# Kernel optimization log

Hardware: AMD Instinct MI355X
Metric: run time of the kernel (lower is better)

The kernel has to match this reference:

```python
import jax, jax.numpy as jnp
import numpy as np
import math

B, N, IN_DIM, OUT_DIM, H = 8, 1024, 256, 256, 8
D_K = OUT_DIM // H


def setup_inputs() -> dict:
    key = jax.random.key(0)
    ks = jax.random.split(key, 12)
    s_in = 1.0 / math.sqrt(IN_DIM)
    s_out = 1.0 / math.sqrt(OUT_DIM)
    return {
        "X": jax.random.normal(ks[0], (B, N, IN_DIM), jnp.float32),
        "A": jax.random.randint(ks[1], (B, N, N), 0, 2, jnp.int32),
        "D": jax.random.uniform(ks[2], (B, N, N), jnp.float32),
        "W_q": jax.random.uniform(ks[3], (IN_DIM, OUT_DIM), jnp.float32, -s_in, s_in),
        "b_q": jax.random.uniform(ks[4], (OUT_DIM,), jnp.float32, -s_in, s_in),
        "W_k": jax.random.uniform(ks[5], (IN_DIM, OUT_DIM), jnp.float32, -s_in, s_in),
        "b_k": jax.random.uniform(ks[6], (OUT_DIM,), jnp.float32, -s_in, s_in),
        "W_v": jax.random.uniform(ks[7], (IN_DIM, OUT_DIM), jnp.float32, -s_in, s_in),
        "b_v": jax.random.uniform(ks[8], (OUT_DIM,), jnp.float32, -s_in, s_in),
        "W_o": jax.random.uniform(ks[9], (OUT_DIM, OUT_DIM), jnp.float32, -s_out, s_out),
        "b_o": jax.random.uniform(ks[10], (OUT_DIM,), jnp.float32, -s_out, s_out),
        "dist_scale": jnp.array(1.0, jnp.float32),
    }


def reference(X, A, D, W_q, b_q, W_k, b_k, W_v, b_v, W_o, b_o, dist_scale):
    b, n, _ = X.shape
    # Projections -> [B, H, N, d_k]
    Q = (X @ W_q + b_q).reshape(b, n, H, D_K).transpose(0, 2, 1, 3)
    K = (X @ W_k + b_k).reshape(b, n, H, D_K).transpose(0, 2, 1, 3)
    V = (X @ W_v + b_v).reshape(b, n, H, D_K).transpose(0, 2, 1, 3)
    scores = jnp.einsum("bhqd,bhkd->bhqk", Q, K) / jnp.sqrt(jnp.float32(D_K))
    scores = scores - dist_scale * D[:, None, :, :]
    scores = jnp.where(A[:, None, :, :] <= 0, jnp.float32(-1e9), scores)
    attn = jax.nn.softmax(scores, axis=-1)  # dropout is identity in eval mode
    out = jnp.einsum("bhqk,bhkd->bhqd", attn, V)
    out = out.transpose(0, 2, 1, 3).reshape(b, n, H * D_K)
    return out @ W_o + b_o
```

## Files before the change

### kernel.cpp

```cpp
#include <hip/hip_runtime.h>


typedef __bf16 bf16x8 __attribute__((ext_vector_type(8)));
typedef float f32x4 __attribute__((ext_vector_type(4)));
typedef int i32x4 __attribute__((ext_vector_type(4)));
typedef unsigned short u16x8 __attribute__((ext_vector_type(8)));
typedef _Float16 f16x8 __attribute__((ext_vector_type(8)));

#define DEV static __device__ __forceinline__

#define LOG2E 1.4426950408889634f
#define QSCALE 0.2550351062f

DEV unsigned short f2bf(float f) {
  union { float f; unsigned u; } x; x.f = f;
  unsigned r = x.u + 0x7fffu + ((x.u >> 16) & 1u);
  return (unsigned short)(r >> 16);
}

DEV unsigned short f2h(float f) {
  _Float16 h = (_Float16)f;
  unsigned short u;
  __builtin_memcpy(&u, &h, 2);
  return u;
}

DEV float h2f(unsigned short u) {
  _Float16 h;
  __builtin_memcpy(&h, &u, 2);
  return (float)h;
}

DEV f32x4 mfma16(bf16x8 a, bf16x8 b, f32x4 c) {
  return __builtin_amdgcn_mfma_f32_16x16x32_bf16(a, b, c, 0, 0, 0);
}

DEV bf16x8 ldfrag(const unsigned short* p) {
  return *reinterpret_cast<const bf16x8*>(p);
}

__global__ __launch_bounds__(256) void k_prep(
    const float* __restrict__ X, const int* __restrict__ A,
    const float* __restrict__ D, const float* __restrict__ dscale,
    const float* __restrict__ Wq, const float* __restrict__ Wk,
    const float* __restrict__ Wv, const float* __restrict__ Wo,
    unsigned short* __restrict__ Xbf, unsigned short* __restrict__ Wt,
    unsigned short* __restrict__ Bias) {
  const int tid = blockIdx.x * 256 + threadIdx.x;
  const int NB4 = (8 * 1024 * 1024) / 4;
  const int NX4 = (8192 * 256) / 4;
  if (tid < NB4) {
    const i32x4 a4 = reinterpret_cast<const i32x4*>(A)[tid];
    const f32x4 d4 = reinterpret_cast<const f32x4*>(D)[tid];
    const float c = -dscale[0] * LOG2E;
    ushort4 o;
    unsigned short* op = (unsigned short*)&o;
    #pragma unroll
    for (int i = 0; i < 4; ++i)
      op[i] = f2h(a4[i] <= 0 ? -60000.0f : c * d4[i]);
    reinterpret_cast<ushort4*>(Bias)[tid] = o;
  } else if (tid < NB4 + NX4) {
    const int t = tid - NB4;
    float4 v = reinterpret_cast<const float4*>(X)[t];
    ushort4 o;
    o.x = f2bf(v.x); o.y = f2bf(v.y); o.z = f2bf(v.z); o.w = f2bf(v.w);
    reinterpret_cast<ushort4*>(Xbf)[t] = o;
  } else {
    int t = tid - NB4 - NX4;
    int mat = t >> 16;
    int e = t & 65535;
    int n = e >> 8, k = e & 255;
    const float* W = (mat == 0) ? Wq : (mat == 1) ? Wk : (mat == 2) ? Wv : Wo;
    Wt[t] = f2bf(W[k * 256 + n]);
  }
}

__global__ __launch_bounds__(256, 2) void k_qkv(
    const unsigned short* __restrict__ Xbf, const unsigned short* __restrict__ Wt,
    const float* __restrict__ bq, const float* __restrict__ bk,
    const float* __restrict__ bv,
    unsigned short* __restrict__ Qb, unsigned short* __restrict__ Kb,
    unsigned short* __restrict__ Vt) {
  const int lane = threadIdx.x & 63;
  const int w = threadIdx.x >> 6;
  const int lr = lane & 15, lg = lane >> 4;
  const int mat = blockIdx.y >> 2;
  const int nloc = (blockIdx.y & 3) * 64 + w * 16;
  const int mbase = blockIdx.x << 8;

  const unsigned short* Wm = Wt + mat * 65536;
  const float* bias = (mat == 0) ? bq : (mat == 1) ? bk : bv;

  bf16x8 bfr[8];
  #pragma unroll
  for (int ks = 0; ks < 8; ++ks)
    bfr[ks] = ldfrag(Wm + (nloc + lr) * 256 + ks * 32 + lg * 8);
  const float bb = bias[nloc + lr];
  const int cm = nloc + lr;
  const int hh = cm >> 5, d = cm & 31;

  for (int mt = 0; mt < 16; ++mt) {
    const int m0 = mbase + mt * 16;
    bf16x8 a[8];
    #pragma unroll
    for (int ks = 0; ks < 8; ++ks)
      a[ks] = ldfrag(Xbf + (m0 + lr) * 256 + ks * 32 + lg * 8);
    f32x4 acc = {0.f, 0.f, 0.f, 0.f};
    #pragma unroll
    for (int ks = 0; ks < 8; ++ks)
      acc = mfma16(a[ks], bfr[ks], acc);

    if (mat == 2) {
      ushort4 vv;
      unsigned short* vp = (unsigned short*)&vv;
      #pragma unroll
      for (int i = 0; i < 4; ++i) vp[i] = f2bf(acc[i] + bb);
      const int row = m0 + lg * 4;
      const int bidx = row >> 10, nn = row & 1023;
      *reinterpret_cast<ushort4*>(&Vt[(((bidx * 8 + hh) * 32) + d) * 1024 + nn]) = vv;
    } else if (mat == 0) {
      #pragma unroll
      for (int i = 0; i < 4; ++i) {
        const int row = m0 + lg * 4 + i;
        const int bidx = row >> 10, nn = row & 1023;
        Qb[(((bidx * 8 + hh) * 1024) + nn) * 32 + d] = f2bf((acc[i] + bb) * QSCALE);
      }
    } else {
      #pragma unroll
      for (int i = 0; i < 4; ++i) {
        const int row = m0 + lg * 4 + i;
        const int bidx = row >> 10, nn = row & 1023;
        Kb[(((bidx * 8 + hh) * 1024) + nn) * 32 + d] = f2bf(acc[i] + bb);
      }
    }
  }
}

__global__ __launch_bounds__(512, 2) void k_attn(
    const unsigned short* __restrict__ Qb, const unsigned short* __restrict__ Kb,
    const unsigned short* __restrict__ Vt, const unsigned short* __restrict__ Bias,
    unsigned short* __restrict__ AO) {
  __shared__ alignas(16) unsigned short Klds[1024 * 32];
  __shared__ alignas(16) unsigned short Vlds[32 * 1024];
  __shared__ alignas(16) unsigned short Sbuf[8][16][72];

  const int tid = threadIdx.x;
  const int lane = tid & 63;
  const int w = tid >> 6;
  const int lr = lane & 15, lg = lane >> 4;
  const int bi = blockIdx.x;
  const int b = bi & 7;
  const int j = bi >> 3;
  const int h = j >> 2, qq = j & 3;
  const int q0w = qq * 256 + w * 32;

  const unsigned short* Kg = Kb + ((size_t)(b * 8 + h) << 15);
  const unsigned short* Vg = Vt + ((size_t)(b * 8 + h) << 15);
  const unsigned short* Qh = Qb + ((size_t)(b * 8 + h) << 15);

  #pragma unroll
  for (int p = 0; p < 8; ++p) {
    const int c = tid + p * 512;
    const int row = c >> 2, seg = c & 3;
    const u16x8 v = *reinterpret_cast<const u16x8*>(Kg + c * 8);
    *reinterpret_cast<u16x8*>(&Klds[row * 32 + ((seg ^ (row & 3)) << 3)]) = v;
  }
  #pragma unroll
  for (int p = 0; p < 8; ++p) {
    const int c = tid + p * 512;
    const int row = c >> 7, ch = c & 127;
    const u16x8 v = *reinterpret_cast<const u16x8*>(Vg + c * 8);
    *reinterpret_cast<u16x8*>(&Vlds[row * 1024 + ((ch ^ (row & 7)) << 3)]) = v;
  }

  bf16x8 qf[2];
  qf[0] = ldfrag(Qh + (q0w + lr) * 32 + lg * 8);
  qf[1] = ldfrag(Qh + (q0w + 16 + lr) * 32 + lg * 8);
  const unsigned short* Br0 = Bias + ((size_t)b << 20) + (size_t)(q0w + lr) * 1024;
  const unsigned short* Br1 = Br0 + (size_t)16 * 1024;

  u16x8 bc[2][2], bn[2][2];
  #pragma unroll
  for (int fr = 0; fr < 2; ++fr) {
    bc[0][fr] = *reinterpret_cast<const u16x8*>(Br0 + fr * 32 + lg * 8);
    bc[1][fr] = *reinterpret_cast<const u16x8*>(Br1 + fr * 32 + lg * 8);
  }

  __syncthreads();

  f32x4 o[2][2];
  #pragma unroll
  for (int s = 0; s < 2; ++s)
    #pragma unroll
    for (int dh = 0; dh < 2; ++dh) o[s][dh] = f32x4{0.f, 0.f, 0.f, 0.f};
  float ps[2] = {0.f, 0.f};

  for (int t = 0; t < 16; ++t) {
    const int k0 = t << 6;
    if (t < 15) {
      #pragma unroll
      for (int fr = 0; fr < 2; ++fr) {
        bn[0][fr] = *reinterpret_cast<const u16x8*>(Br0 + k0 + 64 + fr * 32 + lg * 8);
        bn[1][fr] = *reinterpret_cast<const u16x8*>(Br1 + k0 + 64 + fr * 32 + lg * 8);
      }
    }

    bf16x8 kf[4];
    #pragma unroll
    for (int st = 0; st < 4; ++st) {
      const int row = k0 + st * 16 + lr;
      kf[st] = *reinterpret_cast<const bf16x8*>(
          &Klds[row * 32 + ((lg ^ (lr & 3)) << 3)]);
    }
    bf16x8 vf[2][2];
    #pragma unroll
    for (int dh = 0; dh < 2; ++dh)
      #pragma unroll
      for (int fr = 0; fr < 2; ++fr) {
        const int row = dh * 16 + lr;
        const int ch = t * 8 + ((fr * 4 + lg) ^ (lr & 7));
        vf[dh][fr] = *reinterpret_cast<const bf16x8*>(&Vlds[row * 1024 + ch * 8]);
      }

    #pragma unroll
    for (int s = 0; s < 2; ++s) {
      const f32x4 zz = {0.f, 0.f, 0.f, 0.f};
      f32x4 sv[4];
      #pragma unroll
      for (int st = 0; st < 4; ++st)
        sv[st] = mfma16(kf[st], qf[s], zz);

      #pragma unroll
      for (int st = 0; st < 4; ++st) {
        ushort4 sw;
        unsigned short* sp = (unsigned short*)&sw;
        #pragma unroll
        for (int i = 0; i < 4; ++i) sp[i] = f2h(sv[st][i]);
        *reinterpret_cast<ushort4*>(&Sbuf[w][lr][st * 16 + lg * 4]) = sw;
      }

      #pragma unroll
      for (int fr = 0; fr < 2; ++fr) {
        const f16x8 sf = *reinterpret_cast<const f16x8*>(&Sbuf[w][lr][fr * 32 + lg * 8]);
        const unsigned short* bp = (const unsigned short*)&bc[s][fr];
        float p8[8];
        float psl = 0.f;
        #pragma unroll
        for (int i = 0; i < 8; ++i) {
          p8[i] = exp2f((float)sf[i] + h2f(bp[i]));
          psl += p8[i];
        }
        ps[s] += psl;
        bf16x8 pf;
        #pragma unroll
        for (int i = 0; i < 8; ++i) pf[i] = (__bf16)p8[i];
        o[s][0] = mfma16(vf[0][fr], pf, o[s][0]);
        o[s][1] = mfma16(vf[1][fr], pf, o[s][1]);
      }
    }

    #pragma unroll
    for (int s = 0; s < 2; ++s)
      #pragma unroll
      for (int fr = 0; fr < 2; ++fr)
        bc[s][fr] = bn[s][fr];
  }

  #pragma unroll
  for (int s = 0; s < 2; ++s) {
    float psum = ps[s];
    psum += __shfl_xor(psum, 16);
    psum += __shfl_xor(psum, 32);
    const float linv = 1.0f / psum;
    ushort4 r0, r1;
    unsigned short* r0p = (unsigned short*)&r0;
    unsigned short* r1p = (unsigned short*)&r1;
    #pragma unroll
    for (int i = 0; i < 4; ++i) {
      r0p[i] = f2bf(o[s][0][i] * linv);
      r1p[i] = f2bf(o[s][1][i] * linv);
    }
    const int row = (b << 10) + q0w + s * 16 + lr;
    *reinterpret_cast<ushort4*>(&AO[row * 256 + h * 32 + lg * 4]) = r0;
    *reinterpret_cast<ushort4*>(&AO[row * 256 + h * 32 + 16 + lg * 4]) = r1;
  }
}

__global__ __launch_bounds__(256, 2) void k_oproj(
    const unsigned short* __restrict__ AO, const unsigned short* __restrict__ Wto,
    const float* __restrict__ bo, float* __restrict__ out) {
  const int lane = threadIdx.x & 63;
  const int w = threadIdx.x >> 6;
  const int lr = lane & 15, lg = lane >> 4;
  const int c0 = blockIdx.y * 64 + w * 16;
  const int mbase = blockIdx.x << 7;

  bf16x8 bfr[8];
  #pragma unroll
  for (int ks = 0; ks < 8; ++ks)
    bfr[ks] = ldfrag(Wto + (c0 + lr) * 256 + ks * 32 + lg * 8);
  const float bb = bo[c0 + lr];

  for (int mt = 0; mt < 8; ++mt) {
    const int m0 = mbase + mt * 16;
    bf16x8 a[8];
    #pragma unroll
    for (int ks = 0; ks < 8; ++ks)
      a[ks] = ldfrag(AO + (m0 + lr) * 256 + ks * 32 + lg * 8);
    f32x4 acc = {0.f, 0.f, 0.f, 0.f};
    #pragma unroll
    for (int ks = 0; ks < 8; ++ks)
      acc = mfma16(a[ks], bfr[ks], acc);
    #pragma unroll
    for (int i = 0; i < 4; ++i) {
      const int row = m0 + lg * 4 + i;
      out[row * 256 + c0 + lr] = acc[i] + bb;
    }
  }
}

extern "C" void kernel_launch(void* const* d_in, const int* in_sizes, int n_in,
                              void* d_out, int out_size, void* d_ws, size_t ws_size,
                              hipStream_t stream) {
  const float* X   = (const float*)d_in[0];
  const int*   A   = (const int*)d_in[1];
  const float* D   = (const float*)d_in[2];
  const float* Wq  = (const float*)d_in[3];
  const float* bq  = (const float*)d_in[4];
  const float* Wk  = (const float*)d_in[5];
  const float* bk  = (const float*)d_in[6];
  const float* Wv  = (const float*)d_in[7];
  const float* bv  = (const float*)d_in[8];
  const float* Wo  = (const float*)d_in[9];
  const float* bo  = (const float*)d_in[10];
  const float* dsc = (const float*)d_in[11];
  float* out = (float*)d_out;

  unsigned short* ws = (unsigned short*)d_ws;
  unsigned short* Xbf  = ws;
  unsigned short* Wt   = ws + 2097152;
  unsigned short* Qb   = ws + 2359296;
  unsigned short* Kb   = ws + 4456448;
  unsigned short* Vt   = ws + 6553600;
  unsigned short* Bias = ws + 8650752;
  unsigned short* AO   = Xbf;

  hipLaunchKernelGGL(k_prep, dim3(11264), dim3(256), 0, stream,
                     X, A, D, dsc, Wq, Wk, Wv, Wo, Xbf, Wt, Bias);
  hipLaunchKernelGGL(k_qkv, dim3(32, 12), dim3(256), 0, stream,
                     Xbf, Wt, bq, bk, bv, Qb, Kb, Vt);
  hipLaunchKernelGGL(k_attn, dim3(256), dim3(512), 0, stream,
                     Qb, Kb, Vt, Bias, AO);
  hipLaunchKernelGGL(k_oproj, dim3(64, 4), dim3(256), 0, stream,
                     AO, Wt + 196608, bo, out);
}
```

Measured before the change: 99.94 us.

## Switch pipeline to fp16 MFMA with packed conversions and MFMA row sums

Moves all intermediates and matrix cores from bf16 to fp16 and replaces manual bf16 rounding with packed cvt_pkrtz conversions. In attention, the score-plus-bias add is done in packed fp16 and the softmax denominator is accumulated by an extra MFMA against a ones vector instead of scalar adds and cross-lane shuffles. This is meant to cut VALU conversion and reduction work in the inner loop. The trade-offs are one extra MFMA per fragment and fp16's narrower range with round-toward-zero conversion, which may cost accuracy.

```diff
diff --git a/kernel.cpp b/kernel.cpp
--- a/kernel.cpp
+++ b/kernel.cpp
@@ -1,22 +1,16 @@
 #include <hip/hip_runtime.h>
 
 
-typedef __bf16 bf16x8 __attribute__((ext_vector_type(8)));
+typedef _Float16 f16x8 __attribute__((ext_vector_type(8)));
+typedef __fp16 h16x2 __attribute__((ext_vector_type(2)));
 typedef float f32x4 __attribute__((ext_vector_type(4)));
 typedef int i32x4 __attribute__((ext_vector_type(4)));
 typedef unsigned short u16x8 __attribute__((ext_vector_type(8)));
-typedef _Float16 f16x8 __attribute__((ext_vector_type(8)));
 
 #define DEV static __device__ __forceinline__
 
 #define LOG2E 1.4426950408889634f
 #define QSCALE 0.2550351062f
-
-DEV unsigned short f2bf(float f) {
-  union { float f; unsigned u; } x; x.f = f;
-  unsigned r = x.u + 0x7fffu + ((x.u >> 16) & 1u);
-  return (unsigned short)(r >> 16);
-}
 
 DEV unsigned short f2h(float f) {
   _Float16 h = (_Float16)f;
@@ -25,18 +19,12 @@
   return u;
 }
 
-DEV float h2f(unsigned short u) {
-  _Float16 h;
-  __builtin_memcpy(&h, &u, 2);
-  return (float)h;
-}
-
-DEV f32x4 mfma16(bf16x8 a, bf16x8 b, f32x4 c) {
-  return __builtin_amdgcn_mfma_f32_16x16x32_bf16(a, b, c, 0, 0, 0);
-}
-
-DEV bf16x8 ldfrag(const unsigned short* p) {
-  return *reinterpret_cast<const bf16x8*>(p);
+DEV f32x4 mfma16h(f16x8 a, f16x8 b, f32x4 c) {
+  return __builtin_amdgcn_mfma_f32_16x16x32_f16(a, b, c, 0, 0, 0);
+}
+
+DEV f16x8 ldfragh(const unsigned short* p) {
+  return *reinterpret_cast<const f16x8*>(p);
 }
 
 __global__ __launch_bounds__(256) void k_prep(
@@ -44,7 +32,7 @@
     const float* __restrict__ D, const float* __restrict__ dscale,
     const float* __restrict__ Wq, const float* __restrict__ Wk,
     const float* __restrict__ Wv, const float* __restrict__ Wo,
-    unsigned short* __restrict__ Xbf, unsigned short* __restrict__ Wt,
+    unsigned short* __restrict__ Xh, unsigned short* __restrict__ Wt,
     unsigned short* __restrict__ Bias) {
   const int tid = blockIdx.x * 256 + threadIdx.x;
   const int NB4 = (8 * 1024 * 1024) / 4;
@@ -62,21 +50,22 @@
   } else if (tid < NB4 + NX4) {
     const int t = tid - NB4;
     float4 v = reinterpret_cast<const float4*>(X)[t];
-    ushort4 o;
-    o.x = f2bf(v.x); o.y = f2bf(v.y); o.z = f2bf(v.z); o.w = f2bf(v.w);
-    reinterpret_cast<ushort4*>(Xbf)[t] = o;
+    union { h16x2 h2[2]; ushort4 u; } o;
+    o.h2[0] = __builtin_amdgcn_cvt_pkrtz(v.x, v.y);
+    o.h2[1] = __builtin_amdgcn_cvt_pkrtz(v.z, v.w);
+    reinterpret_cast<ushort4*>(Xh)[t] = o.u;
   } else {
     int t = tid - NB4 - NX4;
     int mat = t >> 16;
     int e = t & 65535;
     int n = e >> 8, k = e & 255;
     const float* W = (mat == 0) ? Wq : (mat == 1) ? Wk : (mat == 2) ? Wv : Wo;
-    Wt[t] = f2bf(W[k * 256 + n]);
+    Wt[t] = f2h(W[k * 256 + n]);
   }
 }
 
 __global__ __launch_bounds__(256, 2) void k_qkv(
-    const unsigned short* __restrict__ Xbf, const unsigned short* __restrict__ Wt,
+    const unsigned short* __restrict__ Xh, const unsigned short* __restrict__ Wt,
     const float* __restrict__ bq, const float* __restrict__ bk,
     const float* __restrict__ bv,
     unsigned short* __restrict__ Qb, unsigned short* __restrict__ Kb,
@@ -91,46 +80,45 @@
   const unsigned short* Wm = Wt + mat * 65536;
   const float* bias = (mat == 0) ? bq : (mat == 1) ? bk : bv;
 
-  bf16x8 bfr[8];
+  f16x8 bfr[8];
   #pragma unroll
   for (int ks = 0; ks < 8; ++ks)
-    bfr[ks] = ldfrag(Wm + (nloc + lr) * 256 + ks * 32 + lg * 8);
+    bfr[ks] = ldfragh(Wm + (nloc + lr) * 256 + ks * 32 + lg * 8);
   const float bb = bias[nloc + lr];
   const int cm = nloc + lr;
   const int hh = cm >> 5, d = cm & 31;
 
   for (int mt = 0; mt < 16; ++mt) {
     const int m0 = mbase + mt * 16;
-    bf16x8 a[8];
+    f16x8 a[8];
     #pragma unroll
     for (int ks = 0; ks < 8; ++ks)
-      a[ks] = ldfrag(Xbf + (m0 + lr) * 256 + ks * 32 + lg * 8);
+      a[ks] = ldfragh(Xh + (m0 + lr) * 256 + ks * 32 + lg * 8);
     f32x4 acc = {0.f, 0.f, 0.f, 0.f};
     #pragma unroll
     for (int ks = 0; ks < 8; ++ks)
-      acc = mfma16(a[ks], bfr[ks], acc);
+      acc = mfma16h(a[ks], bfr[ks], acc);
 
     if (mat == 2) {
-      ushort4 vv;
-      unsigned short* vp = (unsigned short*)&vv;
-      #pragma unroll
-      for (int i = 0; i < 4; ++i) vp[i] = f2bf(acc[i] + bb);
+      union { h16x2 h2[2]; ushort4 u; } vv;
+      vv.h2[0] = __builtin_amdgcn_cvt_pkrtz(acc[0] + bb, acc[1] + bb);
+      vv.h2[1] = __builtin_amdgcn_cvt_pkrtz(acc[2] + bb, acc[3] + bb);
       const int row = m0 + lg * 4;
       const int bidx = row >> 10, nn = row & 1023;
-      *reinterpret_cast<ushort4*>(&Vt[(((bidx * 8 + hh) * 32) + d) * 1024 + nn]) = vv;
+      *reinterpret_cast<ushort4*>(&Vt[(((bidx * 8 + hh) * 32) + d) * 1024 + nn]) = vv.u;
     } else if (mat == 0) {
       #pragma unroll
       for (int i = 0; i < 4; ++i) {
         const int row = m0 + lg * 4 + i;
         const int bidx = row >> 10, nn = row & 1023;
-        Qb[(((bidx * 8 + hh) * 1024) + nn) * 32 + d] = f2bf((acc[i] + bb) * QSCALE);
+        Qb[(((bidx * 8 + hh) * 1024) + nn) * 32 + d] = f2h((acc[i] + bb) * QSCALE);
       }
     } else {
       #pragma unroll
       for (int i = 0; i < 4; ++i) {
         const int row = m0 + lg * 4 + i;
         const int bidx = row >> 10, nn = row & 1023;
-        Kb[(((bidx * 8 + hh) * 1024) + nn) * 32 + d] = f2bf(acc[i] + bb);
+        Kb[(((bidx * 8 + hh) * 1024) + nn) * 32 + d] = f2h(acc[i] + bb);
       }
     }
   }
@@ -173,9 +161,9 @@
     *reinterpret_cast<u16x8*>(&Vlds[row * 1024 + ((ch ^ (row & 7)) << 3)]) = v;
   }
 
-  bf16x8 qf[2];
-  qf[0] = ldfrag(Qh + (q0w + lr) * 32 + lg * 8);
-  qf[1] = ldfrag(Qh + (q0w + 16 + lr) * 32 + lg * 8);
+  f16x8 qf[2];
+  qf[0] = ldfragh(Qh + (q0w + lr) * 32 + lg * 8);
+  qf[1] = ldfragh(Qh + (q0w + 16 + lr) * 32 + lg * 8);
   const unsigned short* Br0 = Bias + ((size_t)b << 20) + (size_t)(q0w + lr) * 1024;
   const unsigned short* Br1 = Br0 + (size_t)16 * 1024;
 
@@ -189,11 +177,16 @@
   __syncthreads();
 
   f32x4 o[2][2];
-  #pragma unroll
-  for (int s = 0; s < 2; ++s)
+  f32x4 lacc[2];
+  #pragma unroll
+  for (int s = 0; s < 2; ++s) {
     #pragma unroll
     for (int dh = 0; dh < 2; ++dh) o[s][dh] = f32x4{0.f, 0.f, 0.f, 0.f};
-  float ps[2] = {0.f, 0.f};
+    lacc[s] = f32x4{0.f, 0.f, 0.f, 0.f};
+  }
+  f16x8 onesv;
+  #pragma unroll
+  for (int i = 0; i < 8; ++i) onesv[i] = (_Float16)1.0f;
 
   for (int t = 0; t < 16; ++t) {
     const int k0 = t << 6;
@@ -205,21 +198,21 @@
       }
     }
 
-    bf16x8 kf[4];
+    f16x8 kf[4];
     #pragma unroll
     for (int st = 0; st < 4; ++st) {
       const int row = k0 + st * 16 + lr;
-      kf[st] = *reinterpret_cast<const bf16x8*>(
+      kf[st] = *reinterpret_cast<const f16x8*>(
           &Klds[row * 32 + ((lg ^ (lr & 3)) << 3)]);
     }
-    bf16x8 vf[2][2];
+    f16x8 vf[2][2];
     #pragma unroll
     for (int dh = 0; dh < 2; ++dh)
       #pragma unroll
       for (int fr = 0; fr < 2; ++fr) {
         const int row = dh * 16 + lr;
         const int ch = t * 8 + ((fr * 4 + lg) ^ (lr & 7));
-        vf[dh][fr] = *reinterpret_cast<const bf16x8*>(&Vlds[row * 1024 + ch * 8]);
+        vf[dh][fr] = *reinterpret_cast<const f16x8*>(&Vlds[row * 1024 + ch * 8]);
       }
 
     #pragma unroll
@@ -228,34 +221,32 @@
       f32x4 sv[4];
       #pragma unroll
       for (int st = 0; st < 4; ++st)
-        sv[st] = mfma16(kf[st], qf[s], zz);
+        sv[st] = mfma16h(kf[st], qf[s], zz);
 
       #pragma unroll
       for (int st = 0; st < 4; ++st) {
-        ushort4 sw;
-        unsigned short* sp = (unsigned short*)&sw;
-        #pragma unroll
-        for (int i = 0; i < 4; ++i) sp[i] = f2h(sv[st][i]);
-        *reinterpret_cast<ushort4*>(&Sbuf[w][lr][st * 16 + lg * 4]) = sw;
+        union { h16x2 h2[2]; ushort4 u; } sw;
+        sw.h2[0] = __builtin_amdgcn_cvt_pkrtz(sv[st][0], sv[st][1]);
+        sw.h2[1] = __builtin_amdgcn_cvt_pkrtz(sv[st][2], sv[st][3]);
+        *reinterpret_cast<ushort4*>(&Sbuf[w][lr][st * 16 + lg * 4]) = sw.u;
       }
 
       #pragma unroll
       for (int fr = 0; fr < 2; ++fr) {
         const f16x8 sf = *reinterpret_cast<const f16x8*>(&Sbuf[w][lr][fr * 32 + lg * 8]);
-        const unsigned short* bp = (const unsigned short*)&bc[s][fr];
-        float p8[8];
-        float psl = 0.f;
+        const f16x8 bfv = *reinterpret_cast<const f16x8*>(&bc[s][fr]);
+        const f16x8 sb = sf + bfv;
+        float e[8];
         #pragma unroll
-        for (int i = 0; i < 8; ++i) {
-          p8[i] = exp2f((float)sf[i] + h2f(bp[i]));
-          psl += p8[i];
-        }
-        ps[s] += psl;
-        bf16x8 pf;
+        for (int i = 0; i < 8; ++i) e[i] = exp2f((float)sb[i]);
+        union { h16x2 h2[4]; f16x8 v; } pfu;
         #pragma unroll
-        for (int i = 0; i < 8; ++i) pf[i] = (__bf16)p8[i];
-        o[s][0] = mfma16(vf[0][fr], pf, o[s][0]);
-        o[s][1] = mfma16(vf[1][fr], pf, o[s][1]);
+        for (int i = 0; i < 4; ++i)
+          pfu.h2[i] = __builtin_amdgcn_cvt_pkrtz(e[2 * i], e[2 * i + 1]);
+        const f16x8 pf = pfu.v;
+        o[s][0] = mfma16h(vf[0][fr], pf, o[s][0]);
+        o[s][1] = mfma16h(vf[1][fr], pf, o[s][1]);
+        lacc[s] = mfma16h(onesv, pf, lacc[s]);
       }
     }
 
@@ -268,17 +259,14 @@
 
   #pragma unroll
   for (int s = 0; s < 2; ++s) {
-    float psum = ps[s];
-    psum += __shfl_xor(psum, 16);
-    psum += __shfl_xor(psum, 32);
-    const float linv = 1.0f / psum;
+    const float linv = 1.0f / lacc[s][0];
     ushort4 r0, r1;
     unsigned short* r0p = (unsigned short*)&r0;
     unsigned short* r1p = (unsigned short*)&r1;
     #pragma unroll
     for (int i = 0; i < 4; ++i) {
-      r0p[i] = f2bf(o[s][0][i] * linv);
-      r1p[i] = f2bf(o[s][1][i] * linv);
+      r0p[i] = f2h(o[s][0][i] * linv);
+      r1p[i] = f2h(o[s][1][i] * linv);
     }
     const int row = (b << 10) + q0w + s * 16 + lr;
     *reinterpret_cast<ushort4*>(&AO[row * 256 + h * 32 + lg * 4]) = r0;
@@ -295,22 +283,22 @@
   const int c0 = blockIdx.y * 64 + w * 16;
   const int mbase = blockIdx.x << 7;
 
-  bf16x8 bfr[8];
+  f16x8 bfr[8];
   #pragma unroll
   for (int ks = 0; ks < 8; ++ks)
-    bfr[ks] = ldfrag(Wto + (c0 + lr) * 256 + ks * 32 + lg * 8);
+    bfr[ks] = ldfragh(Wto + (c0 + lr) * 256 + ks * 32 + lg * 8);
   const float bb = bo[c0 + lr];
 
   for (int mt = 0; mt < 8; ++mt) {
     const int m0 = mbase + mt * 16;
-    bf16x8 a[8];
+    f16x8 a[8];
     #pragma unroll
     for (int ks = 0; ks < 8; ++ks)
-      a[ks] = ldfrag(AO + (m0 + lr) * 256 + ks * 32 + lg * 8);
+      a[ks] = ldfragh(AO + (m0 + lr) * 256 + ks * 32 + lg * 8);
     f32x4 acc = {0.f, 0.f, 0.f, 0.f};
     #pragma unroll
     for (int ks = 0; ks < 8; ++ks)
-      acc = mfma16(a[ks], bfr[ks], acc);
+      acc = mfma16h(a[ks], bfr[ks], acc);
     #pragma unroll
     for (int i = 0; i < 4; ++i) {
       const int row = m0 + lg * 4 + i;
@@ -337,18 +325,18 @@
   float* out = (float*)d_out;
 
   unsigned short* ws = (unsigned short*)d_ws;
-  unsigned short* Xbf  = ws;
+  unsigned short* Xh   = ws;
   unsigned short* Wt   = ws + 2097152;
   unsigned short* Qb   = ws + 2359296;
   unsigned short* Kb   = ws + 4456448;
   unsigned short* Vt   = ws + 6553600;
   unsigned short* Bias = ws + 8650752;
-  unsigned short* AO   = Xbf;
+  unsigned short* AO   = Xh;
 
   hipLaunchKernelGGL(k_prep, dim3(11264), dim3(256), 0, stream,
-                     X, A, D, dsc, Wq, Wk, Wv, Wo, Xbf, Wt, Bias);
+                     X, A, D, dsc, Wq, Wk, Wv, Wo, Xh, Wt, Bias);
   hipLaunchKernelGGL(k_qkv, dim3(32, 12), dim3(256), 0, stream,
-                     Xbf, Wt, bq, bk, bv, Qb, Kb, Vt);
+                     Xh, Wt, bq, bk, bv, Qb, Kb, Vt);
   hipLaunchKernelGGL(k_attn, dim3(256), dim3(512), 0, stream,
                      Qb, Kb, Vt, Bias, AO);
   hipLaunchKernelGGL(k_oproj, dim3(64, 4), dim3(256), 0, stream,
```

After: 88.91 us. 11.0% less time.
